# Kernel tuning notes

Measured on AMD Instinct MI355X. Metric: run time of the kernel, lower is better.

The kernel has to match this reference:

```python
import jax, jax.numpy as jnp
import numpy as np

T = 5       # fixed temporal factor in the original forward
HEADS = 8
DIM = 512
DIM_HEAD = 64
INNER = HEADS * DIM_HEAD  # 512 (must equal DIM for the masked scatter)


def setup_inputs() -> dict:
    key = jax.random.key(0)
    ks = jax.random.split(key, 8)
    bt, n = 40, 3137  # b=8, t=5; n-1 = 56*56 visual tokens
    x = jax.random.normal(ks[0], (bt, n, DIM), dtype=jnp.float32)
    mask = jax.random.randint(ks[1], (bt, 56, 56), 0, 2).astype(jnp.float32)
    s = 1.0 / np.sqrt(DIM)
    w_vq = jax.random.normal(ks[2], (DIM, INNER), dtype=jnp.float32) * s
    w_vkv = jax.random.normal(ks[3], (DIM, 2 * INNER), dtype=jnp.float32) * s
    w_aqkv = jax.random.normal(ks[4], (DIM, 3 * INNER), dtype=jnp.float32) * s
    w_out = jax.random.normal(ks[5], (INNER, DIM), dtype=jnp.float32) * s
    b_out = jnp.zeros((DIM,), dtype=jnp.float32)
    return {"x": x, "mask": mask, "w_vq": w_vq, "w_vkv": w_vkv,
            "w_aqkv": w_aqkv, "w_out": w_out, "b_out": b_out}


def reference(x, mask, w_vq, w_vkv, w_aqkv, w_out, b_out):
    bt, n, dim = x.shape
    b = bt // T
    nv = n - 1
    dh = DIM_HEAD
    scale = dh ** -0.5

    A = x[:, 0]        # (bt, dim) -- single 'action' token per frame
    V = x[:, 1:]       # (bt, nv, dim)
    m = mask.reshape(bt, nv, 1)

    aq, ak, av = jnp.split(A @ w_aqkv, 3, axis=-1)      # each (bt, INNER)
    vk, vv = jnp.split(V @ w_vkv, 2, axis=-1)           # each (bt, nv, INNER)
    vq = V @ w_vq                                        # (bt, nv, INNER)

    # --- A -> V cross attention: per batch, T A-queries over T*nv V keys ---
    qa = aq.reshape(b, T, HEADS, dh)
    Kv = vk.reshape(b, T * nv, HEADS, dh)
    Vv = vv.reshape(b, T * nv, HEADS, dh)
    av_dots = jnp.einsum('bqhd,bkhd->bhqk', qa, Kv) * scale
    av_attn = jax.nn.softmax(av_dots, axis=-1)
    av_o = jnp.einsum('bhqk,bkhd->bqhd', av_attn, Vv)   # (b, T, H, dh)
    a_out = av_o.reshape(bt, 1, INNER)

    # --- V -> A cross attention with block mask: every V token attends only
    # to its own batch's T A-tokens (the -inf block fill in the original) ---
    Qv = vq.reshape(b, T, nv, HEADS, dh)
    Ka = ak.reshape(b, T, HEADS, dh)
    Va = av.reshape(b, T, HEADS, dh)
    va_dots = jnp.einsum('bfnhd,bkhd->bhfnk', Qv, Ka) * scale
    va_attn = jax.nn.softmax(va_dots, axis=-1)          # softmax over T keys
    va_o = jnp.einsum('bhfnk,bkhd->bfnhd', va_attn, Va)
    v_full = va_o.reshape(bt, nv, INNER)

    # original: scatter attn out into V.clone() then * mask, under no_grad()
    # => masked positions get attention output, others V*0 = 0; detached.
    v_out = jax.lax.stop_gradient(v_full * m)

    out = jnp.concatenate([a_out, v_out], axis=1)       # (bt, n, INNER)
    return out @ w_out + b_out
```

## Files before the change

### kernel.cpp

```cpp
#include <hip/hip_runtime.h>

typedef unsigned short u16;
typedef unsigned int u32;
typedef __attribute__((ext_vector_type(8))) u16 u16x8;
typedef __attribute__((ext_vector_type(8))) __bf16 bf16x8;
typedef __attribute__((ext_vector_type(4))) float f32x4;

__device__ __forceinline__ float b2f(u16 u){ return __uint_as_float(((u32)u)<<16); }
__device__ __forceinline__ u16 f2b(float f){
  u32 b = __float_as_uint(f);
  return (u16)((b + 0x7fffu + ((b>>16)&1u))>>16);
}
__device__ __forceinline__ void gload16(const void* g, void* l){
  __builtin_amdgcn_global_load_lds((__attribute__((address_space(1))) void*)g,
                                   (__attribute__((address_space(3))) void*)l, 16, 0, 0);
}
__device__ __forceinline__ float wred_max(float v){
#pragma unroll
  for (int o=32;o>0;o>>=1) v = fmaxf(v, __shfl_xor(v,o));
  return v;
}
__device__ __forceinline__ float wred_sum(float v){
#pragma unroll
  for (int o=32;o>0;o>>=1) v += __shfl_xor(v,o);
  return v;
}

__global__ void k_cast_x(const float* __restrict__ x, u16* __restrict__ xb, int n8){
  int stride = gridDim.x*blockDim.x;
  for (int i = blockIdx.x*blockDim.x + threadIdx.x; i < n8; i += stride){
    const float4* p = (const float4*)(x + (size_t)i*8);
    float4 a = p[0], b = p[1];
    u16x8 o;
    o[0]=f2b(a.x); o[1]=f2b(a.y); o[2]=f2b(a.z); o[3]=f2b(a.w);
    o[4]=f2b(b.x); o[5]=f2b(b.y); o[6]=f2b(b.z); o[7]=f2b(b.w);
    *(u16x8*)(xb + (size_t)i*8) = o;
  }
}

__global__ void k_prep_w(const float* __restrict__ wvq, const float* __restrict__ wvkv,
                         const float* __restrict__ wout, u16* __restrict__ W1T,
                         u16* __restrict__ WoutT){
  int id = blockIdx.x*blockDim.x + threadIdx.x;
  if (id < 786432){
    int n = id >> 9, k = id & 511;
    float v = (n < 512) ? wvq[k*512 + n] : wvkv[k*1024 + (n-512)];
    W1T[id] = f2b(v);
  } else {
    int j = id - 786432;
    int n = j >> 9, k = j & 511;
    WoutT[j] = f2b(wout[k*512 + n]);
  }
}

__global__ void k_agent_qkv(const float* __restrict__ x, const float* __restrict__ w,
                            float* __restrict__ aqkv){
  int id = blockIdx.x*blockDim.x + threadIdx.x;
  int bt = id / 1536, c = id % 1536;
  const float* xr = x + (size_t)bt*3137*512;
  float s = 0.f;
  for (int k=0;k<512;k++) s += xr[k]*w[k*1536+c];
  aqkv[id] = s;
}

template<int FOUT>
__global__ __launch_bounds__(512, 2) void k_gemm256(
    const u16* __restrict__ A, const u16* __restrict__ BT,
    int M, int N, int K, int NX,
    u16* __restrict__ Cb, float* __restrict__ Cf, const float* __restrict__ bias)
{
  __shared__ __align__(16) char Ls[4][32768];
  const int tid = threadIdx.x;
  const int wid = tid >> 6, lane = tid & 63;
  const int nwg = gridDim.x, orig = blockIdx.x;
  const int q8 = nwg >> 3, r8 = nwg & 7;
  const int xc = orig & 7, sl = orig >> 3;
  const int work = (xc < r8 ? xc*(q8+1) : r8*(q8+1) + (xc-r8)*q8) + sl;
  const int m0 = (work / NX) * 256, n0 = (work % NX) * 256;
  const size_t K2 = (size_t)K * 2;
  const char* Ab = (const char*)A;
  const char* Bb = (const char*)BT;
  size_t asrc[2], bsrc[2];
  const int ad0 = wid*1024, ad1 = 8192 + wid*1024;
#pragma unroll
  for (int i=0;i<2;i++){
    int row = (i*8 + wid)*16 + (lane & 15);
    int koff = (lane >> 4) << 4;
    int ra = m0 + row; if (ra >= M) ra = M - 1;
    asrc[i] = (size_t)ra * K2 + koff;
    bsrc[i] = (size_t)(n0 + row) * K2 + koff;
  }
#define STAGE(s4, ks) { \
    size_t ko = (size_t)(ks) * 64; \
    gload16(Ab + asrc[0] + ko, Ls[s4] + ad0); \
    gload16(Ab + asrc[1] + ko, Ls[s4] + ad1); \
    gload16(Bb + bsrc[0] + ko, Ls[s4] + 16384 + ad0); \
    gload16(Bb + bsrc[1] + ko, Ls[s4] + 16384 + ad1); }

  f32x4 acc[8][4] = {};
  const int awb = (wid >> 2) * 8192;
  const int bwb = 16384 + (wid & 3) * 4096;
  const int NS = K >> 5;
  STAGE(0,0) STAGE(1,1) STAGE(2,2)
  for (int s = 0; s < NS; ++s){
    if (s + 2 < NS)      { asm volatile("s_waitcnt vmcnt(8)" ::: "memory"); }
    else if (s + 1 < NS) { asm volatile("s_waitcnt vmcnt(4)" ::: "memory"); }
    else                 { asm volatile("s_waitcnt vmcnt(0)" ::: "memory"); }
    __builtin_amdgcn_s_barrier();
    __builtin_amdgcn_sched_barrier(0);
    if (s + 3 < NS) STAGE((s+3)&3, s+3)
    const char* base = Ls[s & 3];
    bf16x8 af[8], bfr[4];
#pragma unroll
    for (int i=0;i<4;i++) af[i] = *(const bf16x8*)(base + awb + i*1024 + lane*16);
#pragma unroll
    for (int i=0;i<4;i++) bfr[i] = *(const bf16x8*)(base + bwb + i*1024 + lane*16);
    asm volatile("s_waitcnt lgkmcnt(0)" ::: "memory");
    __builtin_amdgcn_sched_barrier(0);
    __builtin_amdgcn_s_setprio(1);
#pragma unroll
    for (int mr=0;mr<4;mr++)
#pragma unroll
      for (int nc=0;nc<4;nc++)
        acc[mr][nc] = __builtin_amdgcn_mfma_f32_16x16x32_bf16(af[mr], bfr[nc], acc[mr][nc], 0,0,0);
    __builtin_amdgcn_s_setprio(0);
#pragma unroll
    for (int i=4;i<8;i++) af[i] = *(const bf16x8*)(base + awb + i*1024 + lane*16);
    asm volatile("s_waitcnt lgkmcnt(0)" ::: "memory");
    __builtin_amdgcn_sched_barrier(0);
    __builtin_amdgcn_s_setprio(1);
#pragma unroll
    for (int mr=4;mr<8;mr++)
#pragma unroll
      for (int nc=0;nc<4;nc++)
        acc[mr][nc] = __builtin_amdgcn_mfma_f32_16x16x32_bf16(af[mr], bfr[nc], acc[mr][nc], 0,0,0);
    __builtin_amdgcn_s_setprio(0);
  }
#undef STAGE
  const int wm = (wid >> 2) * 128, wn = (wid & 3) * 64;
  if (m0 + 256 <= M){
#pragma unroll
    for (int mr=0;mr<8;mr++){
#pragma unroll
      for (int nc=0;nc<4;nc++){
#pragma unroll
        for (int rg=0;rg<4;rg++){
          int row = m0 + wm + mr*16 + ((lane>>4)<<2) + rg;
          int col = n0 + wn + nc*16 + (lane&15);
          float v = acc[mr][nc][rg];
          if (FOUT) Cf[(size_t)row*N + col] = v + bias[col];
          else      Cb[(size_t)row*N + col] = f2b(v);
        }
      }
    }
  } else {
#pragma unroll
    for (int mr=0;mr<8;mr++){
#pragma unroll
      for (int nc=0;nc<4;nc++){
#pragma unroll
        for (int rg=0;rg<4;rg++){
          int row = m0 + wm + mr*16 + ((lane>>4)<<2) + rg;
          int col = n0 + wn + nc*16 + (lane&15);
          if (row < M){
            float v = acc[mr][nc][rg];
            if (FOUT) Cf[(size_t)row*N + col] = v + bias[col];
            else      Cb[(size_t)row*N + col] = f2b(v);
          }
        }
      }
    }
  }
}

__global__ __launch_bounds__(320) void k_attn_agent(
    const u16* __restrict__ out1, const float* __restrict__ aqkv,
    float* __restrict__ pm, float* __restrict__ pl, float* __restrict__ pacc)
{
  __shared__ __align__(16) char Ksm[16384];
  __shared__ __align__(16) char Vsm[16384];
  const int bid = blockIdx.x;
  const int sp = bid & 15, bh = bid >> 4, b = bh >> 3, h = bh & 7;
  const int tid = threadIdx.x, wid = tid >> 6, lane = tid & 63;
  const int q = wid;
  float qreg[64];
  {
    const float* ap = aqkv + ((size_t)(b*5+q)*1536 + h*64);
#pragma unroll
    for (int d=0; d<64; d++) qreg[d] = ap[d];
  }
  float m = -1e30f, l = 0.f;
  float acc[8] = {0,0,0,0,0,0,0,0};
  const int g0 = sp * 980;
  for (int c = 0; c < 8; c++){
    for (int idx = tid; idx < 2048; idx += 320){
      int arr = idx >> 10, rem = idx & 1023;
      int r = rem >> 3, seg = rem & 7;
      int loc = c*128 + r; if (loc > 979) loc = 979;
      int gk = g0 + loc;
      int tk = gk / 3136, nv = gk - tk*3136;
      size_t grow = (size_t)((b*5+tk)*3137 + 1 + nv)*1536 + (arr ? 1024 : 512) + h*64 + seg*8;
      u16x8 v = *(const u16x8*)(out1 + grow);
      char* dst = arr ? Vsm : Ksm;
      *(u16x8*)(dst + r*128 + ((seg*16) ^ ((r&7)<<4))) = v;
    }
    __syncthreads();
    float s0 = 0.f, s1 = 0.f;
#pragma unroll
    for (int seg=0; seg<8; seg++){
      const int r0 = lane, r1 = 64 + lane;
      u16x8 k0 = *(const u16x8*)(Ksm + r0*128 + ((seg*16) ^ ((r0&7)<<4)));
      u16x8 k1 = *(const u16x8*)(Ksm + r1*128 + ((seg*16) ^ ((r1&7)<<4)));
#pragma unroll
      for (int j=0;j<8;j++){
        s0 += qreg[seg*8+j]*b2f(k0[j]);
        s1 += qreg[seg*8+j]*b2f(k1[j]);
      }
    }
    s0 *= 0.125f; s1 *= 0.125f;
    const int locbase = c*128;
    if (locbase + lane >= 980)      s0 = -1e30f;
    if (locbase + 64 + lane >= 980) s1 = -1e30f;
    float cmax = wred_max(fmaxf(s0, s1));
    float mn = fmaxf(m, cmax);
    float resc = __expf(m - mn);
    float p0 = (s0 > -1e29f) ? __expf(s0 - mn) : 0.f;
    float p1 = (s1 > -1e29f) ? __expf(s1 - mn) : 0.f;
    l = l*resc + wred_sum(p0 + p1);
#pragma unroll
    for (int j=0;j<8;j++) acc[j] *= resc;
    const int g = lane >> 3, cc = lane & 7;
#pragma unroll
    for (int i=0;i<16;i++){
      int k = i*8 + g;
      u16x8 vv = *(const u16x8*)(Vsm + k*128 + ((cc*16) ^ ((k&7)<<4)));
      float p = (i < 8) ? __shfl(p0, k) : __shfl(p1, k-64);
#pragma unroll
      for (int j=0;j<8;j++) acc[j] += p*b2f(vv[j]);
    }
    m = mn;
    __syncthreads();
  }
#pragma unroll
  for (int j=0;j<8;j++){
    float v = acc[j];
    v += __shfl_xor(v, 8); v += __shfl_xor(v, 16); v += __shfl_xor(v, 32);
    acc[j] = v;
  }
  const int base = (bh*16 + sp)*5 + q;
  if (lane == 0){ pm[base] = m; pl[base] = l; }
  if (lane < 8){
    float* pa = pacc + (size_t)base*64 + lane*8;
#pragma unroll
    for (int j=0;j<8;j++) pa[j] = acc[j];
  }
}

__global__ void k_agent_combine(const float* __restrict__ pm, const float* __restrict__ pl,
                                const float* __restrict__ pacc, u16* __restrict__ IN)
{
  const int id = blockIdx.x;
  const int q = id % 5, t2 = id / 5;
  const int h = t2 & 7, b = t2 >> 3;
  const int d = threadIdx.x;
  const int bh = b*8 + h;
  float ms = -1e30f;
#pragma unroll
  for (int s2=0;s2<16;s2++) ms = fmaxf(ms, pm[(bh*16+s2)*5+q]);
  float L = 0.f, o = 0.f;
#pragma unroll
  for (int s2=0;s2<16;s2++){
    int base = (bh*16+s2)*5+q;
    float w = __expf(pm[base]-ms);
    L += w*pl[base];
    o += w*pacc[(size_t)base*64 + d];
  }
  IN[(size_t)(b*5+q)*3137*512 + h*64 + d] = f2b(o / L);
}

__global__ __launch_bounds__(256) void k_attn_frame(
    const u16* __restrict__ out1, const float* __restrict__ aqkv,
    const float* __restrict__ mask, u16* __restrict__ IN)
{
  __shared__ float Ka[5][8][68];
  __shared__ float Va[5][8][68];
  const int b = blockIdx.y;
  const int tid = threadIdx.x;
  for (int i = tid; i < 2560; i += 256){
    int t = i >> 9, rem = i & 511, hh = rem >> 6, d = rem & 63;
    const float* src = aqkv + (size_t)(b*5+t)*1536;
    Ka[t][hh][d] = src[512 + hh*64 + d];
    Va[t][hh][d] = src[1024 + hh*64 + d];
  }
  __syncthreads();
  const int task = blockIdx.x*256 + tid;
  const int h = task & 7, rl = task >> 3;
  const int f = rl / 3136, nv = rl - f*3136;
  const int bt = b*5 + f;
  const size_t r1 = (size_t)bt*3137 + 1 + nv;
  const u16* qp = out1 + r1*1536 + h*64;
  float qf[64];
#pragma unroll
  for (int sg=0; sg<8; sg++){
    u16x8 v = *(const u16x8*)(qp + sg*8);
#pragma unroll
    for (int j=0;j<8;j++) qf[sg*8+j] = b2f(v[j]);
  }
  float sd[5];
#pragma unroll
  for (int t=0;t<5;t++){
    float s = 0.f;
#pragma unroll
    for (int d=0;d<64;d++) s += qf[d]*Ka[t][h][d];
    sd[t] = s*0.125f;
  }
  float mx = sd[0];
#pragma unroll
  for (int t=1;t<5;t++) mx = fmaxf(mx, sd[t]);
  float p[5], ps = 0.f;
#pragma unroll
  for (int t=0;t<5;t++){ p[t] = __expf(sd[t]-mx); ps += p[t]; }
  const float mv = mask[(size_t)bt*3136 + nv] / ps;
  u16* op = IN + r1*512 + h*64;
#pragma unroll
  for (int sg=0; sg<8; sg++){
    u16x8 o;
#pragma unroll
    for (int j=0;j<8;j++){
      const int d = sg*8+j;
      float v = 0.f;
#pragma unroll
      for (int t=0;t<5;t++) v += p[t]*Va[t][h][d];
      o[j] = f2b(v*mv);
    }
    *(u16x8*)(op + sg*8) = o;
  }
}

extern "C" void kernel_launch(void* const* d_in, const int* in_sizes, int n_in,
                              void* d_out, int out_size, void* d_ws, size_t ws_size,
                              hipStream_t stream)
{
  const float* x      = (const float*)d_in[0];
  const float* mask   = (const float*)d_in[1];
  const float* w_vq   = (const float*)d_in[2];
  const float* w_vkv  = (const float*)d_in[3];
  const float* w_aqkv = (const float*)d_in[4];
  const float* w_out  = (const float*)d_in[5];
  const float* b_out  = (const float*)d_in[6];
  float* out = (float*)d_out;
  char* ws = (char*)d_ws;

  constexpr size_t MR = 125480;
  constexpr size_t OFF_XB   = 0;
  constexpr size_t OFF_OUT1 = OFF_XB + MR*512*2;
  constexpr size_t OFF_W1T  = OFF_OUT1 + MR*1536*2;
  constexpr size_t OFF_WOT  = OFF_W1T + 1536*512*2;
  constexpr size_t OFF_AQKV = OFF_WOT + 512*512*2;
  constexpr size_t OFF_PM   = OFF_W1T;
  constexpr size_t OFF_PL   = OFF_PM + 5120*4;
  constexpr size_t OFF_PACC = OFF_PL + 5120*4;

  u16* Xb     = (u16*)(ws + OFF_XB);
  u16* out1   = (u16*)(ws + OFF_OUT1);
  u16* W1T    = (u16*)(ws + OFF_W1T);
  u16* WoutT  = (u16*)(ws + OFF_WOT);
  float* aqkv = (float*)(ws + OFF_AQKV);
  float* pm   = (float*)(ws + OFF_PM);
  float* pl   = (float*)(ws + OFF_PL);
  float* pacc = (float*)(ws + OFF_PACC);

  k_cast_x<<<2048, 256, 0, stream>>>(x, Xb, 8030720);
  k_prep_w<<<4096, 256, 0, stream>>>(w_vq, w_vkv, w_out, W1T, WoutT);
  k_agent_qkv<<<240, 256, 0, stream>>>(x, w_aqkv, aqkv);
  k_gemm256<0><<<2946, 512, 0, stream>>>(Xb, W1T, (int)MR, 1536, 512, 6, out1, nullptr, nullptr);
  k_attn_agent<<<1024, 320, 0, stream>>>(out1, aqkv, pm, pl, pacc);
  k_attn_frame<<<dim3(490,8), 256, 0, stream>>>(out1, aqkv, mask, Xb);
  k_agent_combine<<<320, 64, 0, stream>>>(pm, pl, pacc, Xb);
  k_gemm256<1><<<982, 512, 0, stream>>>(Xb, WoutT, (int)MR, 512, 512, 2, nullptr, out, b_out);
}
```

Baseline: 811.7 us.

## Shrink GEMM tiles to 128x128 and merge small prep/combine kernels

The 256x256 four-stage GEMM is replaced with a 128x128 tile, 256-thread, double-buffered variant that uses less LDS, allows more workgroups per CU, and yields a much larger grid. The x cast, weight transposes and agent QKV projection are fused into one launch, and the agent combine step is folded into the frame-attention launch as extra blocks. The pm/pl/pacc buffers are moved off the W1T region, since W1T is now written by the same launch that runs concurrently. Smaller tiles reduce per-tile reuse and add global traffic, and the extra barrier per k-step lowers pipelining depth.

```diff
diff --git a/kernel.cpp b/kernel.cpp
--- a/kernel.cpp
+++ b/kernel.cpp
@@ -26,95 +26,98 @@
   return v;
 }
 
-__global__ void k_cast_x(const float* __restrict__ x, u16* __restrict__ xb, int n8){
-  int stride = gridDim.x*blockDim.x;
-  for (int i = blockIdx.x*blockDim.x + threadIdx.x; i < n8; i += stride){
-    const float4* p = (const float4*)(x + (size_t)i*8);
-    float4 a = p[0], b = p[1];
-    u16x8 o;
-    o[0]=f2b(a.x); o[1]=f2b(a.y); o[2]=f2b(a.z); o[3]=f2b(a.w);
-    o[4]=f2b(b.x); o[5]=f2b(b.y); o[6]=f2b(b.z); o[7]=f2b(b.w);
-    *(u16x8*)(xb + (size_t)i*8) = o;
-  }
-}
-
-__global__ void k_prep_w(const float* __restrict__ wvq, const float* __restrict__ wvkv,
-                         const float* __restrict__ wout, u16* __restrict__ W1T,
-                         u16* __restrict__ WoutT){
-  int id = blockIdx.x*blockDim.x + threadIdx.x;
-  if (id < 786432){
-    int n = id >> 9, k = id & 511;
-    float v = (n < 512) ? wvq[k*512 + n] : wvkv[k*1024 + (n-512)];
-    W1T[id] = f2b(v);
+__global__ void k_pre(const float* __restrict__ x, const float* __restrict__ wvq,
+                      const float* __restrict__ wvkv, const float* __restrict__ wout,
+                      const float* __restrict__ waqkv,
+                      u16* __restrict__ xb, u16* __restrict__ W1T,
+                      u16* __restrict__ WoutT, float* __restrict__ aqkv){
+  const int bid = blockIdx.x, tid = threadIdx.x;
+  if (bid < 2048){
+    const int stride = 2048*256;
+    for (int i = bid*256 + tid; i < 8030720; i += stride){
+      const float4* p = (const float4*)(x + (size_t)i*8);
+      float4 a = p[0], b = p[1];
+      u16x8 o;
+      o[0]=f2b(a.x); o[1]=f2b(a.y); o[2]=f2b(a.z); o[3]=f2b(a.w);
+      o[4]=f2b(b.x); o[5]=f2b(b.y); o[6]=f2b(b.z); o[7]=f2b(b.w);
+      *(u16x8*)(xb + (size_t)i*8) = o;
+    }
+  } else if (bid < 6144){
+    int id = (bid-2048)*256 + tid;
+    if (id < 786432){
+      int n = id >> 9, k = id & 511;
+      float v = (n < 512) ? wvq[k*512 + n] : wvkv[k*1024 + (n-512)];
+      W1T[id] = f2b(v);
+    } else {
+      int j = id - 786432;
+      int n = j >> 9, k = j & 511;
+      WoutT[j] = f2b(wout[k*512 + n]);
+    }
   } else {
-    int j = id - 786432;
-    int n = j >> 9, k = j & 511;
-    WoutT[j] = f2b(wout[k*512 + n]);
-  }
-}
-
-__global__ void k_agent_qkv(const float* __restrict__ x, const float* __restrict__ w,
-                            float* __restrict__ aqkv){
-  int id = blockIdx.x*blockDim.x + threadIdx.x;
-  int bt = id / 1536, c = id % 1536;
-  const float* xr = x + (size_t)bt*3137*512;
-  float s = 0.f;
-  for (int k=0;k<512;k++) s += xr[k]*w[k*1536+c];
-  aqkv[id] = s;
+    int id = (bid-6144)*256 + tid;
+    int bt = id / 1536, c = id % 1536;
+    const float* xr = x + (size_t)bt*3137*512;
+    float s = 0.f;
+    for (int k=0;k<512;k++) s += xr[k]*waqkv[k*1536+c];
+    aqkv[id] = s;
+  }
 }
 
 template<int FOUT>
-__global__ __launch_bounds__(512, 2) void k_gemm256(
+__global__ __launch_bounds__(256, 4) void k_gemm128(
     const u16* __restrict__ A, const u16* __restrict__ BT,
     int M, int N, int K, int NX,
     u16* __restrict__ Cb, float* __restrict__ Cf, const float* __restrict__ bias)
 {
-  __shared__ __align__(16) char Ls[4][32768];
+  __shared__ __align__(16) char Ls[2][16384];
   const int tid = threadIdx.x;
   const int wid = tid >> 6, lane = tid & 63;
   const int nwg = gridDim.x, orig = blockIdx.x;
   const int q8 = nwg >> 3, r8 = nwg & 7;
   const int xc = orig & 7, sl = orig >> 3;
   const int work = (xc < r8 ? xc*(q8+1) : r8*(q8+1) + (xc-r8)*q8) + sl;
-  const int m0 = (work / NX) * 256, n0 = (work % NX) * 256;
+  const int m0 = (work / NX) * 128, n0 = (work % NX) * 128;
   const size_t K2 = (size_t)K * 2;
   const char* Ab = (const char*)A;
   const char* Bb = (const char*)BT;
   size_t asrc[2], bsrc[2];
-  const int ad0 = wid*1024, ad1 = 8192 + wid*1024;
+  const int ad0 = (2*wid)*1024, ad1 = (2*wid+1)*1024;
 #pragma unroll
   for (int i=0;i<2;i++){
-    int row = (i*8 + wid)*16 + (lane & 15);
+    int row = (2*wid + i)*16 + (lane & 15);
     int koff = (lane >> 4) << 4;
-    int ra = m0 + row; if (ra >= M) ra = M - 1;
-    asrc[i] = (size_t)ra * K2 + koff;
-    bsrc[i] = (size_t)(n0 + row) * K2 + koff;
-  }
-#define STAGE(s4, ks) { \
+    int ra = m0 + row; if (ra >= M) ra = M-1;
+    asrc[i] = (size_t)ra*K2 + koff;
+    bsrc[i] = (size_t)(n0 + row)*K2 + koff;
+  }
+#define STAGE(s2, ks) { \
     size_t ko = (size_t)(ks) * 64; \
-    gload16(Ab + asrc[0] + ko, Ls[s4] + ad0); \
-    gload16(Ab + asrc[1] + ko, Ls[s4] + ad1); \
-    gload16(Bb + bsrc[0] + ko, Ls[s4] + 16384 + ad0); \
-    gload16(Bb + bsrc[1] + ko, Ls[s4] + 16384 + ad1); }
-
-  f32x4 acc[8][4] = {};
-  const int awb = (wid >> 2) * 8192;
-  const int bwb = 16384 + (wid & 3) * 4096;
+    gload16(Ab + asrc[0] + ko, Ls[s2] + ad0); \
+    gload16(Ab + asrc[1] + ko, Ls[s2] + ad1); \
+    gload16(Bb + bsrc[0] + ko, Ls[s2] + 8192 + ad0); \
+    gload16(Bb + bsrc[1] + ko, Ls[s2] + 8192 + ad1); }
+
+  f32x4 acc[4][4] = {};
+  const int awb = (wid>>1)*4096;
+  const int bwb = 8192 + (wid&1)*4096;
   const int NS = K >> 5;
-  STAGE(0,0) STAGE(1,1) STAGE(2,2)
+  STAGE(0,0)
   for (int s = 0; s < NS; ++s){
-    if (s + 2 < NS)      { asm volatile("s_waitcnt vmcnt(8)" ::: "memory"); }
-    else if (s + 1 < NS) { asm volatile("s_waitcnt vmcnt(4)" ::: "memory"); }
-    else                 { asm volatile("s_waitcnt vmcnt(0)" ::: "memory"); }
+    if (s+1 < NS){
+      STAGE((s+1)&1, s+1)
+      asm volatile("s_waitcnt vmcnt(4)" ::: "memory");
+    } else {
+      asm volatile("s_waitcnt vmcnt(0)" ::: "memory");
+    }
     __builtin_amdgcn_s_barrier();
     __builtin_amdgcn_sched_barrier(0);
-    if (s + 3 < NS) STAGE((s+3)&3, s+3)
-    const char* base = Ls[s & 3];
-    bf16x8 af[8], bfr[4];
+    const char* base = Ls[s&1];
+    bf16x8 af[4], bf[4];
 #pragma unroll
     for (int i=0;i<4;i++) af[i] = *(const bf16x8*)(base + awb + i*1024 + lane*16);
 #pragma unroll
-    for (int i=0;i<4;i++) bfr[i] = *(const bf16x8*)(base + bwb + i*1024 + lane*16);
+    for (int i=0;i<4;i++) bf[i] = *(const bf16x8*)(base + bwb + i*1024 + lane*16);
+    __builtin_amdgcn_sched_barrier(0);
     asm volatile("s_waitcnt lgkmcnt(0)" ::: "memory");
     __builtin_amdgcn_sched_barrier(0);
     __builtin_amdgcn_s_setprio(1);
@@ -122,25 +125,16 @@
     for (int mr=0;mr<4;mr++)
 #pragma unroll
       for (int nc=0;nc<4;nc++)
-        acc[mr][nc] = __builtin_amdgcn_mfma_f32_16x16x32_bf16(af[mr], bfr[nc], acc[mr][nc], 0,0,0);
+        acc[mr][nc] = __builtin_amdgcn_mfma_f32_16x16x32_bf16(af[mr], bf[nc], acc[mr][nc], 0,0,0);
     __builtin_amdgcn_s_setprio(0);
-#pragma unroll
-    for (int i=4;i<8;i++) af[i] = *(const bf16x8*)(base + awb + i*1024 + lane*16);
-    asm volatile("s_waitcnt lgkmcnt(0)" ::: "memory");
     __builtin_amdgcn_sched_barrier(0);
-    __builtin_amdgcn_s_setprio(1);
-#pragma unroll
-    for (int mr=4;mr<8;mr++)
-#pragma unroll
-      for (int nc=0;nc<4;nc++)
-        acc[mr][nc] = __builtin_amdgcn_mfma_f32_16x16x32_bf16(af[mr], bfr[nc], acc[mr][nc], 0,0,0);
-    __builtin_amdgcn_s_setprio(0);
+    __builtin_amdgcn_s_barrier();
   }
 #undef STAGE
-  const int wm = (wid >> 2) * 128, wn = (wid & 3) * 64;
-  if (m0 + 256 <= M){
-#pragma unroll
-    for (int mr=0;mr<8;mr++){
+  const int wm = (wid>>1)*64, wn = (wid&1)*64;
+  if (m0 + 128 <= M){
+#pragma unroll
+    for (int mr=0;mr<4;mr++){
 #pragma unroll
       for (int nc=0;nc<4;nc++){
 #pragma unroll
@@ -155,7 +149,7 @@
     }
   } else {
 #pragma unroll
-    for (int mr=0;mr<8;mr++){
+    for (int mr=0;mr<4;mr++){
 #pragma unroll
       for (int nc=0;nc<4;nc++){
 #pragma unroll
@@ -256,84 +250,84 @@
   }
 }
 
-__global__ void k_agent_combine(const float* __restrict__ pm, const float* __restrict__ pl,
-                                const float* __restrict__ pacc, u16* __restrict__ IN)
-{
-  const int id = blockIdx.x;
-  const int q = id % 5, t2 = id / 5;
-  const int h = t2 & 7, b = t2 >> 3;
-  const int d = threadIdx.x;
-  const int bh = b*8 + h;
-  float ms = -1e30f;
-#pragma unroll
-  for (int s2=0;s2<16;s2++) ms = fmaxf(ms, pm[(bh*16+s2)*5+q]);
-  float L = 0.f, o = 0.f;
-#pragma unroll
-  for (int s2=0;s2<16;s2++){
-    int base = (bh*16+s2)*5+q;
-    float w = __expf(pm[base]-ms);
-    L += w*pl[base];
-    o += w*pacc[(size_t)base*64 + d];
-  }
-  IN[(size_t)(b*5+q)*3137*512 + h*64 + d] = f2b(o / L);
-}
-
 __global__ __launch_bounds__(256) void k_attn_frame(
     const u16* __restrict__ out1, const float* __restrict__ aqkv,
-    const float* __restrict__ mask, u16* __restrict__ IN)
+    const float* __restrict__ mask, const float* __restrict__ pm,
+    const float* __restrict__ pl, const float* __restrict__ pacc,
+    u16* __restrict__ IN)
 {
-  __shared__ float Ka[5][8][68];
-  __shared__ float Va[5][8][68];
-  const int b = blockIdx.y;
-  const int tid = threadIdx.x;
-  for (int i = tid; i < 2560; i += 256){
-    int t = i >> 9, rem = i & 511, hh = rem >> 6, d = rem & 63;
-    const float* src = aqkv + (size_t)(b*5+t)*1536;
-    Ka[t][hh][d] = src[512 + hh*64 + d];
-    Va[t][hh][d] = src[1024 + hh*64 + d];
-  }
-  __syncthreads();
-  const int task = blockIdx.x*256 + tid;
-  const int h = task & 7, rl = task >> 3;
-  const int f = rl / 3136, nv = rl - f*3136;
-  const int bt = b*5 + f;
-  const size_t r1 = (size_t)bt*3137 + 1 + nv;
-  const u16* qp = out1 + r1*1536 + h*64;
-  float qf[64];
-#pragma unroll
-  for (int sg=0; sg<8; sg++){
-    u16x8 v = *(const u16x8*)(qp + sg*8);
-#pragma unroll
-    for (int j=0;j<8;j++) qf[sg*8+j] = b2f(v[j]);
-  }
-  float sd[5];
-#pragma unroll
-  for (int t=0;t<5;t++){
-    float s = 0.f;
-#pragma unroll
-    for (int d=0;d<64;d++) s += qf[d]*Ka[t][h][d];
-    sd[t] = s*0.125f;
-  }
-  float mx = sd[0];
-#pragma unroll
-  for (int t=1;t<5;t++) mx = fmaxf(mx, sd[t]);
-  float p[5], ps = 0.f;
-#pragma unroll
-  for (int t=0;t<5;t++){ p[t] = __expf(sd[t]-mx); ps += p[t]; }
-  const float mv = mask[(size_t)bt*3136 + nv] / ps;
-  u16* op = IN + r1*512 + h*64;
-#pragma unroll
-  for (int sg=0; sg<8; sg++){
-    u16x8 o;
-#pragma unroll
-    for (int j=0;j<8;j++){
-      const int d = sg*8+j;
-      float v = 0.f;
-#pragma unroll
-      for (int t=0;t<5;t++) v += p[t]*Va[t][h][d];
-      o[j] = f2b(v*mv);
-    }
-    *(u16x8*)(op + sg*8) = o;
+  const int bid = blockIdx.x, tid = threadIdx.x;
+  if (bid < 3920){
+    __shared__ float Ka[5][8][68];
+    __shared__ float Va[5][8][68];
+    const int b = bid / 490, bx = bid % 490;
+    for (int i = tid; i < 2560; i += 256){
+      int t = i >> 9, rem = i & 511, hh = rem >> 6, d = rem & 63;
+      const float* src = aqkv + (size_t)(b*5+t)*1536;
+      Ka[t][hh][d] = src[512 + hh*64 + d];
+      Va[t][hh][d] = src[1024 + hh*64 + d];
+    }
+    __syncthreads();
+    const int task = bx*256 + tid;
+    const int h = task & 7, rl = task >> 3;
+    const int f = rl / 3136, nv = rl - f*3136;
+    const int bt = b*5 + f;
+    const size_t r1 = (size_t)bt*3137 + 1 + nv;
+    const u16* qp = out1 + r1*1536 + h*64;
+    float qf[64];
+#pragma unroll
+    for (int sg=0; sg<8; sg++){
+      u16x8 v = *(const u16x8*)(qp + sg*8);
+#pragma unroll
+      for (int j=0;j<8;j++) qf[sg*8+j] = b2f(v[j]);
+    }
+    float sd[5];
+#pragma unroll
+    for (int t=0;t<5;t++){
+      float s = 0.f;
+#pragma unroll
+      for (int d=0;d<64;d++) s += qf[d]*Ka[t][h][d];
+      sd[t] = s*0.125f;
+    }
+    float mx = sd[0];
+#pragma unroll
+    for (int t=1;t<5;t++) mx = fmaxf(mx, sd[t]);
+    float p[5], ps = 0.f;
+#pragma unroll
+    for (int t=0;t<5;t++){ p[t] = __expf(sd[t]-mx); ps += p[t]; }
+    const float mv = mask[(size_t)bt*3136 + nv] / ps;
+    u16* op = IN + r1*512 + h*64;
+#pragma unroll
+    for (int sg=0; sg<8; sg++){
+      u16x8 o;
+#pragma unroll
+      for (int j=0;j<8;j++){
+        const int d = sg*8+j;
+        float v = 0.f;
+#pragma unroll
+        for (int t=0;t<5;t++) v += p[t]*Va[t][h][d];
+        o[j] = f2b(v*mv);
+      }
+      *(u16x8*)(op + sg*8) = o;
+    }
+  } else {
+    const int id = (bid - 3920)*4 + (tid >> 6);
+    const int d = tid & 63;
+    const int q = id % 5, t2 = id / 5;
+    const int h = t2 & 7, b = t2 >> 3;
+    const int bh = b*8 + h;
+    float ms = -1e30f;
+#pragma unroll
+    for (int s2=0;s2<16;s2++) ms = fmaxf(ms, pm[(bh*16+s2)*5+q]);
+    float L = 0.f, o = 0.f;
+#pragma unroll
+    for (int s2=0;s2<16;s2++){
+      int base = (bh*16+s2)*5+q;
+      float w = __expf(pm[base]-ms);
+      L += w*pl[base];
+      o += w*pacc[(size_t)base*64 + d];
+    }
+    IN[(size_t)(b*5+q)*3137*512 + h*64 + d] = f2b(o / L);
   }
 }
 
@@ -357,7 +351,7 @@
   constexpr size_t OFF_W1T  = OFF_OUT1 + MR*1536*2;
   constexpr size_t OFF_WOT  = OFF_W1T + 1536*512*2;
   constexpr size_t OFF_AQKV = OFF_WOT + 512*512*2;
-  constexpr size_t OFF_PM   = OFF_W1T;
+  constexpr size_t OFF_PM   = OFF_AQKV + 40*1536*4;
   constexpr size_t OFF_PL   = OFF_PM + 5120*4;
   constexpr size_t OFF_PACC = OFF_PL + 5120*4;
 
@@ -370,12 +364,9 @@
   float* pl   = (float*)(ws + OFF_PL);
   float* pacc = (float*)(ws + OFF_PACC);
 
-  k_cast_x<<<2048, 256, 0, stream>>>(x, Xb, 8030720);
-  k_prep_w<<<4096, 256, 0, stream>>>(w_vq, w_vkv, w_out, W1T, WoutT);
-  k_agent_qkv<<<240, 256, 0, stream>>>(x, w_aqkv, aqkv);
-  k_gemm256<0><<<2946, 512, 0, stream>>>(Xb, W1T, (int)MR, 1536, 512, 6, out1, nullptr, nullptr);
+  k_pre<<<6384, 256, 0, stream>>>(x, w_vq, w_vkv, w_out, w_aqkv, Xb, W1T, WoutT, aqkv);
+  k_gemm128<0><<<11772, 256, 0, stream>>>(Xb, W1T, (int)MR, 1536, 512, 12, out1, nullptr, nullptr);
   k_attn_agent<<<1024, 320, 0, stream>>>(out1, aqkv, pm, pl, pacc);
-  k_attn_frame<<<dim3(490,8), 256, 0, stream>>>(out1, aqkv, mask, Xb);
-  k_agent_combine<<<320, 64, 0, stream>>>(pm, pl, pacc, Xb);
-  k_gemm256<1><<<982, 512, 0, stream>>>(Xb, WoutT, (int)MR, 512, 512, 2, nullptr, out, b_out);
-}
+  k_attn_frame<<<4000, 256, 0, stream>>>(out1, aqkv, mask, pm, pl, pacc, Xb);
+  k_gemm128<1><<<3924, 256, 0, stream>>>(Xb, WoutT, (int)MR, 512, 512, 4, nullptr, out, b_out);
+}
```

Result: slower. 928.1 us (+14.3%).
